# Optimization experiments

Measured on AMD Instinct MI355X. Metric: run time of the kernel, lower is better.

## Reference

```python
import jax, jax.numpy as jnp
import numpy as np

TOP_K = 2

def setup_inputs() -> dict:
    key = jax.random.key(0)
    ks = jax.random.split(key, 7)
    B, L, D, H, E, S = 2, 2048, 1024, 512, 16, 2048
    s = lambda fan_in: (1.0 / np.sqrt(fan_in)).astype(np.float32)
    return {
        "x": jax.random.normal(ks[0], (B, L, D), jnp.float32),
        "gate_w": jax.random.normal(ks[1], (E, D), jnp.float32) * s(D),
        "w1": jax.random.normal(ks[2], (E, H, D), jnp.float32) * s(D),
        "w2": jax.random.normal(ks[3], (E, D, H), jnp.float32) * s(H),
        "sfc1": jax.random.normal(ks[4], (S, D), jnp.float32) * s(D),
        "sfc2": jax.random.normal(ks[5], (S, D), jnp.float32) * s(D),
        "sfc3": jax.random.normal(ks[6], (D, S), jnp.float32) * s(S),
    }

def reference(x, gate_w, w1, w2, sfc1, sfc2, sfc3):
    B, L, D = x.shape
    E = gate_w.shape[0]
    # shared expert: SwiGLU MLP
    shared = jnp.einsum("bls,ds->bld", jax.nn.silu(jnp.einsum("bld,sd->bls", x, sfc1)) * jnp.einsum("bld,sd->bls", x, sfc2), sfc3)
    # router: top-k over gate logits, softmax over selected logits only
    logits = jnp.einsum("bld,ed->ble", x, gate_w)
    top_w, top_idx = jax.lax.top_k(logits, TOP_K)           # [B,L,K]
    top_w = jax.nn.softmax(top_w, axis=-1)
    xf = x.reshape(-1, D)                                    # [T,D]
    T = xf.shape[0]
    idx = top_idx.reshape(T, TOP_K)
    wk = top_w.reshape(T, TOP_K)
    # dense combine weights [T,E]: routing weight where selected, else 0
    dispatch = jnp.zeros((T, E), xf.dtype).at[jnp.arange(T)[:, None], idx].add(wk)
    # all-expert dense compute, combined with dispatch weights (avoids [T,E,D])
    h = jax.nn.silu(jnp.einsum("td,ehd->teh", xf, w1))       # [T,E,H]
    moe = jnp.einsum("teh,te,edh->td", h, dispatch, w2)      # [T,D]
    return moe.reshape(B, L, D) + shared
```

## Files before the change

### kernel.cpp

```cpp
#include <hip/hip_runtime.h>
#include <stdint.h>

#define T_TOK 4096
#define D_DIM 1024
#define H_DIM 512
#define E_NUM 16
#define S_DIM 2048

#define DUAL_BLOCKS 512
#define MOE1_TILES_MAX 80
#define SHOUT_BLOCKS 256

typedef __attribute__((ext_vector_type(8))) __bf16 bf16x8;
typedef __attribute__((ext_vector_type(4))) float f32x4;

__device__ __forceinline__ uint16_t f2bf(float f) {
  uint32_t u = __float_as_uint(f);
  u += 0x7fffu + ((u >> 16) & 1u);
  return (uint16_t)(u >> 16);
}

__device__ __forceinline__ float bf2f(uint16_t u) {
  return __uint_as_float(((uint32_t)u) << 16);
}

__device__ __forceinline__ float silu_f(float v) {
  return v / (1.f + __expf(-v));
}

#define N4_X (T_TOK * D_DIM / 4)
#define N4_S (S_DIM * D_DIM / 4)
#define N4_W (E_NUM * H_DIM * D_DIM / 4)
#define N4_TOT (N4_X + 3 * N4_S + 2 * N4_W)

__global__ __launch_bounds__(256) void k_cast_all(
    const float* __restrict__ x, const float* __restrict__ sfc1,
    const float* __restrict__ sfc2, const float* __restrict__ sfc3,
    const float* __restrict__ w1, const float* __restrict__ w2,
    uint16_t* __restrict__ xb, uint16_t* __restrict__ s1b,
    uint16_t* __restrict__ s2b, uint16_t* __restrict__ s3b,
    uint16_t* __restrict__ w1b, uint16_t* __restrict__ w2b) {
  int i = blockIdx.x * 256 + threadIdx.x;
  if (i >= N4_TOT) return;
  const float* src; uint16_t* dst; int off;
  if (i < N4_X)                    { src = x;    dst = xb;  off = 0; }
  else if (i < N4_X + N4_S)        { src = sfc1; dst = s1b; off = N4_X; }
  else if (i < N4_X + 2 * N4_S)    { src = sfc2; dst = s2b; off = N4_X + N4_S; }
  else if (i < N4_X + 3 * N4_S)    { src = sfc3; dst = s3b; off = N4_X + 2 * N4_S; }
  else if (i < N4_X + 3 * N4_S + N4_W) { src = w1; dst = w1b; off = N4_X + 3 * N4_S; }
  else                             { src = w2;  dst = w2b; off = N4_X + 3 * N4_S + N4_W; }
  int j = i - off;
  float4 v = ((const float4*)src)[j];
  ushort4 o;
  o.x = f2bf(v.x); o.y = f2bf(v.y); o.z = f2bf(v.z); o.w = f2bf(v.w);
  ((ushort4*)dst)[j] = o;
}

__global__ void k_gwT(const float* __restrict__ gw, float4* __restrict__ gwT4) {
  int tid = blockIdx.x * 256 + threadIdx.x;
  if (tid >= E_NUM * (D_DIM / 4)) return;
  int k4 = tid & (D_DIM / 4 - 1);
  int e = tid >> 8;
  float4 v = ((const float4*)(gw + (size_t)e * D_DIM))[k4];
  gwT4[(size_t)k4 * E_NUM + e] = v;
}

__global__ __launch_bounds__(256) void k_router(
    const float* __restrict__ x, const float4* __restrict__ gwT4,
    int* __restrict__ top_idx, float* __restrict__ top_w) {
  const int wid = threadIdx.x >> 6, lane = threadIdx.x & 63;
  const int t = blockIdx.x * 4 + wid;
  const int e = lane & 15, q = lane >> 4;
  const float4* xr4 = (const float4*)(x + (size_t)t * D_DIM) + q * 64;
  const float4* g4 = gwT4 + (size_t)q * 64 * E_NUM + e;
  float acc = 0.f;
#pragma unroll 8
  for (int i = 0; i < 64; i++) {
    float4 xv = xr4[i];
    float4 gv = g4[(size_t)i * E_NUM];
    acc += xv.x * gv.x + xv.y * gv.y + xv.z * gv.z + xv.w * gv.w;
  }
  acc += __shfl_xor(acc, 16, 64);
  acc += __shfl_xor(acc, 32, 64);
  float v1 = acc; int i1 = e;
#pragma unroll
  for (int off = 1; off < 16; off <<= 1) {
    float ov = __shfl_xor(v1, off, 64);
    int oi = __shfl_xor(i1, off, 64);
    if (ov > v1 || (ov == v1 && oi < i1)) { v1 = ov; i1 = oi; }
  }
  float v2 = (e == i1) ? -1e30f : acc; int i2 = e;
#pragma unroll
  for (int off = 1; off < 16; off <<= 1) {
    float ov = __shfl_xor(v2, off, 64);
    int oi = __shfl_xor(i2, off, 64);
    if (ov > v2 || (ov == v2 && oi < i2)) { v2 = ov; i2 = oi; }
  }
  if (lane == 0) {
    float w0 = 1.f / (1.f + __expf(v2 - v1));
    top_idx[t * 2] = i1; top_idx[t * 2 + 1] = i2;
    top_w[t * 2] = w0;  top_w[t * 2 + 1] = 1.f - w0;
  }
}

__global__ __launch_bounds__(256) void k_hist(const int* __restrict__ top_idx,
                                              int* __restrict__ partial) {
  __shared__ int h[E_NUM];
  int tid = threadIdx.x;
  if (tid < E_NUM) h[tid] = 0;
  __syncthreads();
  int id = blockIdx.x * 256 + tid;
  atomicAdd(&h[top_idx[id]], 1);
  __syncthreads();
  if (tid < E_NUM) partial[blockIdx.x * E_NUM + tid] = h[tid];
}

__global__ void k_scan(const int* __restrict__ partial, int* __restrict__ bases,
                       int* __restrict__ offsets, int* __restrict__ tile_e,
                       int* __restrict__ tile_m, int* __restrict__ tile_cnt) {
  __shared__ int tot[E_NUM];
  int e = threadIdx.x;
  if (e < E_NUM) {
    int run = 0;
    for (int b = 0; b < 32; b++) { bases[b * E_NUM + e] = run; run += partial[b * E_NUM + e]; }
    tot[e] = run;
  }
  __syncthreads();
  if (e == 0) {
    int s = 0;
    for (int i = 0; i < E_NUM; i++) { offsets[i] = s; s += tot[i]; }
    offsets[E_NUM] = s;
    int cnt = 0;
    for (int i = 0; i < E_NUM; i++)
      for (int m0 = 0; m0 < tot[i]; m0 += 128) { tile_e[cnt] = i; tile_m[cnt] = m0; cnt++; }
    tile_cnt[0] = cnt;
  }
  __syncthreads();
  if (e < E_NUM) {
    int off = offsets[e];
    for (int b = 0; b < 32; b++) bases[b * E_NUM + e] += off;
  }
}

__global__ __launch_bounds__(256) void k_scatter(
    const int* __restrict__ top_idx, const float* __restrict__ top_w,
    const int* __restrict__ bases, int* __restrict__ slot_token,
    float* __restrict__ slot_w, int* __restrict__ slot_of) {
  __shared__ int cur[E_NUM];
  int tid = threadIdx.x;
  if (tid < E_NUM) cur[tid] = bases[blockIdx.x * E_NUM + tid];
  __syncthreads();
  int id = blockIdx.x * 256 + tid;
  int e = top_idx[id];
  int slot = atomicAdd(&cur[e], 1);
  slot_token[slot] = id >> 1;
  slot_w[slot] = top_w[id];
  slot_of[id] = slot;
}

__global__ __launch_bounds__(256) void k_stage1(
    const uint16_t* __restrict__ xb, const uint16_t* __restrict__ b1,
    const uint16_t* __restrict__ b2, uint16_t* __restrict__ hs,
    const uint16_t* __restrict__ w1b, const int* __restrict__ offsets,
    const int* __restrict__ slot_token, const int* __restrict__ tile_e,
    const int* __restrict__ tile_m, const int* __restrict__ tile_cnt,
    uint16_t* __restrict__ hbuf) {
  __shared__ uint16_t smem[6 * 4096];
  const int bid = blockIdx.x;
  const int tid = threadIdx.x, lane = tid & 63, wid = tid >> 6;
  const int wm = wid >> 1, wn = wid & 1;
  const int r = lane & 15, q = lane >> 4;
  const int row0 = tid >> 2, col8 = (tid & 3) * 8;
  const int st0 = tid * 8, st1 = 2048 + tid * 8;

  if (bid < DUAL_BLOCKS) {
    const int bn0 = (bid & 15) * 128, bm0 = (bid >> 4) * 128;
    uint16_t* sA = smem;
    uint16_t* sB1 = smem + 8192;
    uint16_t* sB2 = smem + 16384;
    f32x4 acc1[4][4], acc2[4][4];
#pragma unroll
    for (int i = 0; i < 4; i++)
#pragma unroll
      for (int j = 0; j < 4; j++) {
        acc1[i][j] = (f32x4){0.f, 0.f, 0.f, 0.f};
        acc2[i][j] = (f32x4){0.f, 0.f, 0.f, 0.f};
      }
    const uint16_t* ga0 = xb + (size_t)(bm0 + row0) * D_DIM + col8;
    const uint16_t* ga1 = ga0 + 64 * D_DIM;
    const uint16_t* gb10 = b1 + (size_t)(bn0 + row0) * D_DIM + col8;
    const uint16_t* gb11 = gb10 + 64 * D_DIM;
    const uint16_t* gb20 = b2 + (size_t)(bn0 + row0) * D_DIM + col8;
    const uint16_t* gb21 = gb20 + 64 * D_DIM;

    uint4 pA0, pA1, pB10, pB11, pB20, pB21;
    pA0 = *(const uint4*)ga0;   pA1 = *(const uint4*)ga1;
    pB10 = *(const uint4*)gb10; pB11 = *(const uint4*)gb11;
    pB20 = *(const uint4*)gb20; pB21 = *(const uint4*)gb21;
    ga0 += 32; ga1 += 32; gb10 += 32; gb11 += 32; gb20 += 32; gb21 += 32;
    *(uint4*)(sA + st0) = pA0;   *(uint4*)(sA + st1) = pA1;
    *(uint4*)(sB1 + st0) = pB10; *(uint4*)(sB1 + st1) = pB11;
    *(uint4*)(sB2 + st0) = pB20; *(uint4*)(sB2 + st1) = pB21;
    __syncthreads();

    int cur = 0;
    for (int kt = 32; kt < D_DIM; kt += 32) {
      pA0 = *(const uint4*)ga0;   pA1 = *(const uint4*)ga1;
      pB10 = *(const uint4*)gb10; pB11 = *(const uint4*)gb11;
      pB20 = *(const uint4*)gb20; pB21 = *(const uint4*)gb21;
      ga0 += 32; ga1 += 32; gb10 += 32; gb11 += 32; gb20 += 32; gb21 += 32;
      {
        const uint16_t* A = sA + cur * 4096;
        const uint16_t* B1 = sB1 + cur * 4096;
        const uint16_t* B2 = sB2 + cur * 4096;
        bf16x8 a[4];
#pragma unroll
        for (int i = 0; i < 4; i++)
          a[i] = *(const bf16x8*)(A + (wm * 64 + i * 16 + r) * 32 + q * 8);
#pragma unroll
        for (int j = 0; j < 4; j++) {
          bf16x8 b = *(const bf16x8*)(B1 + (wn * 64 + j * 16 + r) * 32 + q * 8);
#pragma unroll
          for (int i = 0; i < 4; i++)
            acc1[i][j] = __builtin_amdgcn_mfma_f32_16x16x32_bf16(a[i], b, acc1[i][j], 0, 0, 0);
        }
#pragma unroll
        for (int j = 0; j < 4; j++) {
          bf16x8 b = *(const bf16x8*)(B2 + (wn * 64 + j * 16 + r) * 32 + q * 8);
#pragma unroll
          for (int i = 0; i < 4; i++)
            acc2[i][j] = __builtin_amdgcn_mfma_f32_16x16x32_bf16(a[i], b, acc2[i][j], 0, 0, 0);
        }
      }
      int nxt = cur ^ 1;
      *(uint4*)(sA + nxt * 4096 + st0) = pA0;   *(uint4*)(sA + nxt * 4096 + st1) = pA1;
      *(uint4*)(sB1 + nxt * 4096 + st0) = pB10; *(uint4*)(sB1 + nxt * 4096 + st1) = pB11;
      *(uint4*)(sB2 + nxt * 4096 + st0) = pB20; *(uint4*)(sB2 + nxt * 4096 + st1) = pB21;
      __syncthreads();
      cur = nxt;
    }
    {
      const uint16_t* A = sA + cur * 4096;
      const uint16_t* B1 = sB1 + cur * 4096;
      const uint16_t* B2 = sB2 + cur * 4096;
      bf16x8 a[4];
#pragma unroll
      for (int i = 0; i < 4; i++)
        a[i] = *(const bf16x8*)(A + (wm * 64 + i * 16 + r) * 32 + q * 8);
#pragma unroll
      for (int j = 0; j < 4; j++) {
        bf16x8 b = *(const bf16x8*)(B1 + (wn * 64 + j * 16 + r) * 32 + q * 8);
#pragma unroll
        for (int i = 0; i < 4; i++)
          acc1[i][j] = __builtin_amdgcn_mfma_f32_16x16x32_bf16(a[i], b, acc1[i][j], 0, 0, 0);
      }
#pragma unroll
      for (int j = 0; j < 4; j++) {
        bf16x8 b = *(const bf16x8*)(B2 + (wn * 64 + j * 16 + r) * 32 + q * 8);
#pragma unroll
        for (int i = 0; i < 4; i++)
          acc2[i][j] = __builtin_amdgcn_mfma_f32_16x16x32_bf16(a[i], b, acc2[i][j], 0, 0, 0);
      }
    }
#pragma unroll
    for (int i = 0; i < 4; i++)
#pragma unroll
      for (int j = 0; j < 4; j++)
#pragma unroll
        for (int rr = 0; rr < 4; rr++) {
          int row = bm0 + wm * 64 + i * 16 + q * 4 + rr;
          int col = bn0 + wn * 64 + j * 16 + r;
          hs[(size_t)row * S_DIM + col] = f2bf(silu_f(acc1[i][j][rr]) * acc2[i][j][rr]);
        }
  } else {
    int idx = bid - DUAL_BLOCKS;
    int t = idx >> 2;
    if (t >= tile_cnt[0]) return;
    const int n0 = (idx & 3) * 128;
    const int e = tile_e[t], m0 = tile_m[t];
    const int base = offsets[e];
    const int ne = offsets[e + 1] - base;
    uint16_t* sA = smem;
    uint16_t* sB = smem + 8192;
    f32x4 acc[4][4];
#pragma unroll
    for (int i = 0; i < 4; i++)
#pragma unroll
      for (int j = 0; j < 4; j++) acc[i][j] = (f32x4){0.f, 0.f, 0.f, 0.f};
    const int e0 = min(m0 + row0, ne - 1);
    const int e1 = min(m0 + row0 + 64, ne - 1);
    const uint16_t* ga0 = xb + (size_t)slot_token[base + e0] * D_DIM + col8;
    const uint16_t* ga1 = xb + (size_t)slot_token[base + e1] * D_DIM + col8;
    const uint16_t* wbase = w1b + (size_t)e * H_DIM * D_DIM;
    const uint16_t* gb0 = wbase + (size_t)(n0 + row0) * D_DIM + col8;
    const uint16_t* gb1 = gb0 + 64 * D_DIM;

    uint4 pA0, pA1, pB0, pB1;
    pA0 = *(const uint4*)ga0; pA1 = *(const uint4*)ga1;
    pB0 = *(const uint4*)gb0; pB1 = *(const uint4*)gb1;
    ga0 += 32; ga1 += 32; gb0 += 32; gb1 += 32;
    *(uint4*)(sA + st0) = pA0; *(uint4*)(sA + st1) = pA1;
    *(uint4*)(sB + st0) = pB0; *(uint4*)(sB + st1) = pB1;
    __syncthreads();

    int cur = 0;
    for (int kt = 32; kt < D_DIM; kt += 32) {
      pA0 = *(const uint4*)ga0; pA1 = *(const uint4*)ga1;
      pB0 = *(const uint4*)gb0; pB1 = *(const uint4*)gb1;
      ga0 += 32; ga1 += 32; gb0 += 32; gb1 += 32;
      {
        const uint16_t* A = sA + cur * 4096;
        const uint16_t* B = sB + cur * 4096;
        bf16x8 a[4], bb[4];
#pragma unroll
        for (int i = 0; i < 4; i++)
          a[i] = *(const bf16x8*)(A + (wm * 64 + i * 16 + r) * 32 + q * 8);
#pragma unroll
        for (int j = 0; j < 4; j++)
          bb[j] = *(const bf16x8*)(B + (wn * 64 + j * 16 + r) * 32 + q * 8);
#pragma unroll
        for (int i = 0; i < 4; i++)
#pragma unroll
          for (int j = 0; j < 4; j++)
            acc[i][j] = __builtin_amdgcn_mfma_f32_16x16x32_bf16(a[i], bb[j], acc[i][j], 0, 0, 0);
      }
      int nxt = cur ^ 1;
      *(uint4*)(sA + nxt * 4096 + st0) = pA0; *(uint4*)(sA + nxt * 4096 + st1) = pA1;
      *(uint4*)(sB + nxt * 4096 + st0) = pB0; *(uint4*)(sB + nxt * 4096 + st1) = pB1;
      __syncthreads();
      cur = nxt;
    }
    {
      const uint16_t* A = sA + cur * 4096;
      const uint16_t* B = sB + cur * 4096;
      bf16x8 a[4], bb[4];
#pragma unroll
      for (int i = 0; i < 4; i++)
        a[i] = *(const bf16x8*)(A + (wm * 64 + i * 16 + r) * 32 + q * 8);
#pragma unroll
      for (int j = 0; j < 4; j++)
        bb[j] = *(const bf16x8*)(B + (wn * 64 + j * 16 + r) * 32 + q * 8);
#pragma unroll
      for (int i = 0; i < 4; i++)
#pragma unroll
        for (int j = 0; j < 4; j++)
          acc[i][j] = __builtin_amdgcn_mfma_f32_16x16x32_bf16(a[i], bb[j], acc[i][j], 0, 0, 0);
    }
#pragma unroll
    for (int i = 0; i < 4; i++)
#pragma unroll
      for (int j = 0; j < 4; j++)
#pragma unroll
        for (int rr = 0; rr < 4; rr++) {
          int ent = m0 + wm * 64 + i * 16 + q * 4 + rr;
          if (ent < ne) {
            int col = n0 + wn * 64 + j * 16 + r;
            hbuf[(size_t)(base + ent) * H_DIM + col] = f2bf(silu_f(acc[i][j][rr]));
          }
        }
  }
}

__global__ __launch_bounds__(256) void k_stage2(
    const uint16_t* __restrict__ hsb, const uint16_t* __restrict__ sfc3b,
    float* __restrict__ out, const uint16_t* __restrict__ hbuf,
    const uint16_t* __restrict__ w2b, const int* __restrict__ offsets,
    const float* __restrict__ slot_w, const int* __restrict__ tile_e,
    const int* __restrict__ tile_m, const int* __restrict__ tile_cnt,
    uint16_t* __restrict__ slot_out) {
  __shared__ uint16_t smem[4 * 4096];
  const int bid = blockIdx.x;
  const int tid = threadIdx.x, lane = tid & 63, wid = tid >> 6;
  const int wm = wid >> 1, wn = wid & 1;
  const int r = lane & 15, q = lane >> 4;
  const int row0 = tid >> 2, col8 = (tid & 3) * 8;
  const int st0 = tid * 8, st1 = 2048 + tid * 8;
  uint16_t* sA = smem;
  uint16_t* sB = smem + 8192;

  if (bid < SHOUT_BLOCKS) {
    const int bn0 = (bid & 7) * 128, bm0 = (bid >> 3) * 128;
    f32x4 acc[4][4];
#pragma unroll
    for (int i = 0; i < 4; i++)
#pragma unroll
      for (int j = 0; j < 4; j++) acc[i][j] = (f32x4){0.f, 0.f, 0.f, 0.f};
    const uint16_t* ga0 = hsb + (size_t)(bm0 + row0) * S_DIM + col8;
    const uint16_t* ga1 = ga0 + (size_t)64 * S_DIM;
    const uint16_t* gb0 = sfc3b + (size_t)(bn0 + row0) * S_DIM + col8;
    const uint16_t* gb1 = gb0 + (size_t)64 * S_DIM;

    uint4 pA0, pA1, pB0, pB1;
    pA0 = *(const uint4*)ga0; pA1 = *(const uint4*)ga1;
    pB0 = *(const uint4*)gb0; pB1 = *(const uint4*)gb1;
    ga0 += 32; ga1 += 32; gb0 += 32; gb1 += 32;
    *(uint4*)(sA + st0) = pA0; *(uint4*)(sA + st1) = pA1;
    *(uint4*)(sB + st0) = pB0; *(uint4*)(sB + st1) = pB1;
    __syncthreads();

    int cur = 0;
    for (int kt = 32; kt < S_DIM; kt += 32) {
      pA0 = *(const uint4*)ga0; pA1 = *(const uint4*)ga1;
      pB0 = *(const uint4*)gb0; pB1 = *(const uint4*)gb1;
      ga0 += 32; ga1 += 32; gb0 += 32; gb1 += 32;
      {
        const uint16_t* A = sA + cur * 4096;
        const uint16_t* B = sB + cur * 4096;
        bf16x8 a[4], bb[4];
#pragma unroll
        for (int i = 0; i < 4; i++)
          a[i] = *(const bf16x8*)(A + (wm * 64 + i * 16 + r) * 32 + q * 8);
#pragma unroll
        for (int j = 0; j < 4; j++)
          bb[j] = *(const bf16x8*)(B + (wn * 64 + j * 16 + r) * 32 + q * 8);
#pragma unroll
        for (int i = 0; i < 4; i++)
#pragma unroll
          for (int j = 0; j < 4; j++)
            acc[i][j] = __builtin_amdgcn_mfma_f32_16x16x32_bf16(a[i], bb[j], acc[i][j], 0, 0, 0);
      }
      int nxt = cur ^ 1;
      *(uint4*)(sA + nxt * 4096 + st0) = pA0; *(uint4*)(sA + nxt * 4096 + st1) = pA1;
      *(uint4*)(sB + nxt * 4096 + st0) = pB0; *(uint4*)(sB + nxt * 4096 + st1) = pB1;
      __syncthreads();
      cur = nxt;
    }
    {
      const uint16_t* A = sA + cur * 4096;
      const uint16_t* B = sB + cur * 4096;
      bf16x8 a[4], bb[4];
#pragma unroll
      for (int i = 0; i < 4; i++)
        a[i] = *(const bf16x8*)(A + (wm * 64 + i * 16 + r) * 32 + q * 8);
#pragma unroll
      for (int j = 0; j < 4; j++)
        bb[j] = *(const bf16x8*)(B + (wn * 64 + j * 16 + r) * 32 + q * 8);
#pragma unroll
      for (int i = 0; i < 4; i++)
#pragma unroll
        for (int j = 0; j < 4; j++)
          acc[i][j] = __builtin_amdgcn_mfma_f32_16x16x32_bf16(a[i], bb[j], acc[i][j], 0, 0, 0);
    }
#pragma unroll
    for (int i = 0; i < 4; i++)
#pragma unroll
      for (int j = 0; j < 4; j++)
#pragma unroll
        for (int rr = 0; rr < 4; rr++) {
          int row = bm0 + wm * 64 + i * 16 + q * 4 + rr;
          int col = bn0 + wn * 64 + j * 16 + r;
          out[(size_t)row * D_DIM + col] = acc[i][j][rr];
        }
  } else {
    int idx = bid - SHOUT_BLOCKS;
    int t = idx >> 3;
    if (t >= tile_cnt[0]) return;
    const int n0 = (idx & 7) * 128;
    const int e = tile_e[t], m0 = tile_m[t];
    const int base = offsets[e];
    const int ne = offsets[e + 1] - base;
    f32x4 acc[4][4];
#pragma unroll
    for (int i = 0; i < 4; i++)
#pragma unroll
      for (int j = 0; j < 4; j++) acc[i][j] = (f32x4){0.f, 0.f, 0.f, 0.f};
    const int e0 = min(m0 + row0, ne - 1);
    const int e1 = min(m0 + row0 + 64, ne - 1);
    const uint16_t* ga0 = hbuf + (size_t)(base + e0) * H_DIM + col8;
    const uint16_t* ga1 = hbuf + (size_t)(base + e1) * H_DIM + col8;
    const uint16_t* wbase = w2b + (size_t)e * D_DIM * H_DIM;
    const uint16_t* gb0 = wbase + (size_t)(n0 + row0) * H_DIM + col8;
    const uint16_t* gb1 = gb0 + 64 * H_DIM;

    uint4 pA0, pA1, pB0, pB1;
    pA0 = *(const uint4*)ga0; pA1 = *(const uint4*)ga1;
    pB0 = *(const uint4*)gb0; pB1 = *(const uint4*)gb1;
    ga0 += 32; ga1 += 32; gb0 += 32; gb1 += 32;
    *(uint4*)(sA + st0) = pA0; *(uint4*)(sA + st1) = pA1;
    *(uint4*)(sB + st0) = pB0; *(uint4*)(sB + st1) = pB1;
    __syncthreads();

    int cur = 0;
    for (int kt = 32; kt < H_DIM; kt += 32) {
      pA0 = *(const uint4*)ga0; pA1 = *(const uint4*)ga1;
      pB0 = *(const uint4*)gb0; pB1 = *(const uint4*)gb1;
      ga0 += 32; ga1 += 32; gb0 += 32; gb1 += 32;
      {
        const uint16_t* A = sA + cur * 4096;
        const uint16_t* B = sB + cur * 4096;
        bf16x8 a[4], bb[4];
#pragma unroll
        for (int i = 0; i < 4; i++)
          a[i] = *(const bf16x8*)(A + (wm * 64 + i * 16 + r) * 32 + q * 8);
#pragma unroll
        for (int j = 0; j < 4; j++)
          bb[j] = *(const bf16x8*)(B + (wn * 64 + j * 16 + r) * 32 + q * 8);
#pragma unroll
        for (int i = 0; i < 4; i++)
#pragma unroll
          for (int j = 0; j < 4; j++)
            acc[i][j] = __builtin_amdgcn_mfma_f32_16x16x32_bf16(a[i], bb[j], acc[i][j], 0, 0, 0);
      }
      int nxt = cur ^ 1;
      *(uint4*)(sA + nxt * 4096 + st0) = pA0; *(uint4*)(sA + nxt * 4096 + st1) = pA1;
      *(uint4*)(sB + nxt * 4096 + st0) = pB0; *(uint4*)(sB + nxt * 4096 + st1) = pB1;
      __syncthreads();
      cur = nxt;
    }
    {
      const uint16_t* A = sA + cur * 4096;
      const uint16_t* B = sB + cur * 4096;
      bf16x8 a[4], bb[4];
#pragma unroll
      for (int i = 0; i < 4; i++)
        a[i] = *(const bf16x8*)(A + (wm * 64 + i * 16 + r) * 32 + q * 8);
#pragma unroll
      for (int j = 0; j < 4; j++)
        bb[j] = *(const bf16x8*)(B + (wn * 64 + j * 16 + r) * 32 + q * 8);
#pragma unroll
      for (int i = 0; i < 4; i++)
#pragma unroll
        for (int j = 0; j < 4; j++)
          acc[i][j] = __builtin_amdgcn_mfma_f32_16x16x32_bf16(a[i], bb[j], acc[i][j], 0, 0, 0);
    }
#pragma unroll
    for (int i = 0; i < 4; i++) {
      int ent_base = m0 + wm * 64 + i * 16 + q * 4;
#pragma unroll
      for (int rr = 0; rr < 4; rr++) {
        int ent = ent_base + rr;
        if (ent < ne) {
          float w = slot_w[base + ent];
          uint16_t* orow = slot_out + (size_t)(base + ent) * D_DIM;
#pragma unroll
          for (int j = 0; j < 4; j++) {
            int col = n0 + wn * 64 + j * 16 + r;
            orow[col] = f2bf(w * acc[i][j][rr]);
          }
        }
      }
    }
  }
}

__global__ __launch_bounds__(256) void k_combine(
    const uint16_t* __restrict__ slot_out, const int* __restrict__ slot_of,
    float* __restrict__ out) {
  int t = blockIdx.x;
  int c = threadIdx.x;
  int s0 = slot_of[t * 2], s1 = slot_of[t * 2 + 1];
  ushort4 a = ((const ushort4*)(slot_out + (size_t)s0 * D_DIM))[c];
  ushort4 b = ((const ushort4*)(slot_out + (size_t)s1 * D_DIM))[c];
  float4* po = (float4*)(out + (size_t)t * D_DIM) + c;
  float4 o = *po;
  o.x += bf2f(a.x) + bf2f(b.x);
  o.y += bf2f(a.y) + bf2f(b.y);
  o.z += bf2f(a.z) + bf2f(b.z);
  o.w += bf2f(a.w) + bf2f(b.w);
  *po = o;
}

extern "C" void kernel_launch(void* const* d_in, const int* in_sizes, int n_in,
                              void* d_out, int out_size, void* d_ws, size_t ws_size,
                              hipStream_t stream) {
  const float* x     = (const float*)d_in[0];
  const float* gatew = (const float*)d_in[1];
  const float* w1    = (const float*)d_in[2];
  const float* w2    = (const float*)d_in[3];
  const float* sfc1  = (const float*)d_in[4];
  const float* sfc2  = (const float*)d_in[5];
  const float* sfc3  = (const float*)d_in[6];
  float* out = (float*)d_out;

  uint8_t* ws = (uint8_t*)d_ws;
  size_t off = 0;
  auto alloc = [&](size_t bytes) {
    void* p = ws + off;
    off = (off + bytes + 255) & ~(size_t)255;
    return p;
  };
  uint16_t* xb    = (uint16_t*)alloc((size_t)T_TOK * D_DIM * 2);
  uint16_t* sfc1b = (uint16_t*)alloc((size_t)S_DIM * D_DIM * 2);
  uint16_t* sfc2b = (uint16_t*)alloc((size_t)S_DIM * D_DIM * 2);
  uint16_t* sfc3b = (uint16_t*)alloc((size_t)D_DIM * S_DIM * 2);
  uint16_t* w1b   = (uint16_t*)alloc((size_t)E_NUM * H_DIM * D_DIM * 2);
  uint16_t* w2b   = (uint16_t*)alloc((size_t)E_NUM * D_DIM * H_DIM * 2);
  uint16_t* hsb   = (uint16_t*)alloc((size_t)T_TOK * S_DIM * 2);
  uint16_t* hbuf  = (uint16_t*)alloc((size_t)2 * T_TOK * H_DIM * 2);
  uint16_t* slot_out = (uint16_t*)alloc((size_t)2 * T_TOK * D_DIM * 2);
  float4* gwT4    = (float4*)alloc((size_t)D_DIM / 4 * E_NUM * 16);
  int*   top_idx  = (int*)alloc((size_t)T_TOK * 2 * 4);
  float* top_w    = (float*)alloc((size_t)T_TOK * 2 * 4);
  int*   partial  = (int*)alloc(32 * E_NUM * 4);
  int*   bases    = (int*)alloc(32 * E_NUM * 4);
  int*   offsets  = (int*)alloc((E_NUM + 1) * 4);
  int*   tile_e   = (int*)alloc(MOE1_TILES_MAX * 4);
  int*   tile_m   = (int*)alloc(MOE1_TILES_MAX * 4);
  int*   tile_cnt = (int*)alloc(4);
  int*   slot_token = (int*)alloc((size_t)2 * T_TOK * 4);
  float* slot_w   = (float*)alloc((size_t)2 * T_TOK * 4);
  int*   slot_of  = (int*)alloc((size_t)2 * T_TOK * 4);

  k_cast_all<<<(N4_TOT + 255) / 256, 256, 0, stream>>>(
      x, sfc1, sfc2, sfc3, w1, w2, xb, sfc1b, sfc2b, sfc3b, w1b, w2b);
  k_gwT<<<(E_NUM * D_DIM / 4 + 255) / 256, 256, 0, stream>>>(gatew, gwT4);
  k_router<<<T_TOK / 4, 256, 0, stream>>>(x, gwT4, top_idx, top_w);
  k_hist<<<32, 256, 0, stream>>>(top_idx, partial);
  k_scan<<<1, 64, 0, stream>>>(partial, bases, offsets, tile_e, tile_m, tile_cnt);
  k_scatter<<<32, 256, 0, stream>>>(top_idx, top_w, bases, slot_token, slot_w, slot_of);
  k_stage1<<<DUAL_BLOCKS + MOE1_TILES_MAX * 4, 256, 0, stream>>>(
      xb, sfc1b, sfc2b, hsb, w1b, offsets, slot_token, tile_e, tile_m, tile_cnt, hbuf);
  k_stage2<<<SHOUT_BLOCKS + MOE1_TILES_MAX * 8, 256, 0, stream>>>(
      hsb, sfc3b, out, hbuf, w2b, offsets, slot_w, tile_e, tile_m, tile_cnt, slot_out);
  k_combine<<<T_TOK, 256, 0, stream>>>(slot_out, slot_of, out);
}
```

Before: 311.1 us.

## Switch GEMMs to 32x32x16 MFMA and merge routing prep kernels

All GEMM paths move from 16x16x32 MFMA tiles to 32x32x16 MFMA with f32x16 accumulators. Each warp now loads fewer LDS fragments per MFMA, and the tail iteration is folded into the main loop. The gate-weight transpose is merged into the cast kernel, and hist/scan/scatter are replaced by a single-block sort kernel, which removes several launches. The cost is that the sort now runs serially in one block. Stage2's shared-expert and MoE branches are unified into one loop.

```diff
diff --git a/kernel.cpp b/kernel.cpp
--- a/kernel.cpp
+++ b/kernel.cpp
@@ -12,7 +12,7 @@
 #define SHOUT_BLOCKS 256
 
 typedef __attribute__((ext_vector_type(8))) __bf16 bf16x8;
-typedef __attribute__((ext_vector_type(4))) float f32x4;
+typedef __attribute__((ext_vector_type(16))) float f32x16;
 
 __device__ __forceinline__ uint16_t f2bf(float f) {
   uint32_t u = __float_as_uint(f);
@@ -32,16 +32,27 @@
 #define N4_S (S_DIM * D_DIM / 4)
 #define N4_W (E_NUM * H_DIM * D_DIM / 4)
 #define N4_TOT (N4_X + 3 * N4_S + 2 * N4_W)
+#define N4_GW (E_NUM * D_DIM / 4)
 
 __global__ __launch_bounds__(256) void k_cast_all(
     const float* __restrict__ x, const float* __restrict__ sfc1,
     const float* __restrict__ sfc2, const float* __restrict__ sfc3,
     const float* __restrict__ w1, const float* __restrict__ w2,
+    const float* __restrict__ gw,
     uint16_t* __restrict__ xb, uint16_t* __restrict__ s1b,
     uint16_t* __restrict__ s2b, uint16_t* __restrict__ s3b,
-    uint16_t* __restrict__ w1b, uint16_t* __restrict__ w2b) {
+    uint16_t* __restrict__ w1b, uint16_t* __restrict__ w2b,
+    float4* __restrict__ gwT4) {
   int i = blockIdx.x * 256 + threadIdx.x;
-  if (i >= N4_TOT) return;
+  if (i >= N4_TOT) {
+    int t = i - N4_TOT;
+    if (t < N4_GW) {
+      int k4 = t & (D_DIM / 4 - 1);
+      int e = t >> 8;
+      gwT4[(size_t)k4 * E_NUM + e] = ((const float4*)(gw + (size_t)e * D_DIM))[k4];
+    }
+    return;
+  }
   const float* src; uint16_t* dst; int off;
   if (i < N4_X)                    { src = x;    dst = xb;  off = 0; }
   else if (i < N4_X + N4_S)        { src = sfc1; dst = s1b; off = N4_X; }
@@ -54,15 +65,6 @@
   ushort4 o;
   o.x = f2bf(v.x); o.y = f2bf(v.y); o.z = f2bf(v.z); o.w = f2bf(v.w);
   ((ushort4*)dst)[j] = o;
-}
-
-__global__ void k_gwT(const float* __restrict__ gw, float4* __restrict__ gwT4) {
-  int tid = blockIdx.x * 256 + threadIdx.x;
-  if (tid >= E_NUM * (D_DIM / 4)) return;
-  int k4 = tid & (D_DIM / 4 - 1);
-  int e = tid >> 8;
-  float4 v = ((const float4*)(gw + (size_t)e * D_DIM))[k4];
-  gwT4[(size_t)k4 * E_NUM + e] = v;
 }
 
 __global__ __launch_bounds__(256) void k_router(
@@ -103,60 +105,41 @@
   }
 }
 
-__global__ __launch_bounds__(256) void k_hist(const int* __restrict__ top_idx,
-                                              int* __restrict__ partial) {
+__global__ __launch_bounds__(256) void k_sort(
+    const int* __restrict__ top_idx, const float* __restrict__ top_w,
+    int* __restrict__ offsets, int* __restrict__ tile_e,
+    int* __restrict__ tile_m, int* __restrict__ tile_cnt,
+    int* __restrict__ slot_token, float* __restrict__ slot_w,
+    int* __restrict__ slot_of) {
   __shared__ int h[E_NUM];
+  __shared__ int offs[E_NUM + 1];
   int tid = threadIdx.x;
   if (tid < E_NUM) h[tid] = 0;
   __syncthreads();
-  int id = blockIdx.x * 256 + tid;
-  atomicAdd(&h[top_idx[id]], 1);
+  for (int i = tid; i < 2 * T_TOK; i += 256) atomicAdd(&h[top_idx[i]], 1);
   __syncthreads();
-  if (tid < E_NUM) partial[blockIdx.x * E_NUM + tid] = h[tid];
-}
-
-__global__ void k_scan(const int* __restrict__ partial, int* __restrict__ bases,
-                       int* __restrict__ offsets, int* __restrict__ tile_e,
-                       int* __restrict__ tile_m, int* __restrict__ tile_cnt) {
-  __shared__ int tot[E_NUM];
-  int e = threadIdx.x;
-  if (e < E_NUM) {
-    int run = 0;
-    for (int b = 0; b < 32; b++) { bases[b * E_NUM + e] = run; run += partial[b * E_NUM + e]; }
-    tot[e] = run;
+  if (tid == 0) {
+    int s = 0;
+    for (int e = 0; e < E_NUM; e++) { offs[e] = s; s += h[e]; }
+    offs[E_NUM] = s;
+    int cnt = 0;
+    for (int e = 0; e < E_NUM; e++)
+      for (int m0 = 0; m0 < h[e]; m0 += 128) { tile_e[cnt] = e; tile_m[cnt] = m0; cnt++; }
+    tile_cnt[0] = cnt;
+    for (int e = 0; e <= E_NUM; e++) offsets[e] = offs[e];
   }
   __syncthreads();
-  if (e == 0) {
-    int s = 0;
-    for (int i = 0; i < E_NUM; i++) { offsets[i] = s; s += tot[i]; }
-    offsets[E_NUM] = s;
-    int cnt = 0;
-    for (int i = 0; i < E_NUM; i++)
-      for (int m0 = 0; m0 < tot[i]; m0 += 128) { tile_e[cnt] = i; tile_m[cnt] = m0; cnt++; }
-    tile_cnt[0] = cnt;
-  }
+  if (tid < E_NUM) h[tid] = offs[tid];
   __syncthreads();
-  if (e < E_NUM) {
-    int off = offsets[e];
-    for (int b = 0; b < 32; b++) bases[b * E_NUM + e] += off;
-  }
-}
-
-__global__ __launch_bounds__(256) void k_scatter(
-    const int* __restrict__ top_idx, const float* __restrict__ top_w,
-    const int* __restrict__ bases, int* __restrict__ slot_token,
-    float* __restrict__ slot_w, int* __restrict__ slot_of) {
-  __shared__ int cur[E_NUM];
-  int tid = threadIdx.x;
-  if (tid < E_NUM) cur[tid] = bases[blockIdx.x * E_NUM + tid];
-  __syncthreads();
-  int id = blockIdx.x * 256 + tid;
-  int e = top_idx[id];
-  int slot = atomicAdd(&cur[e], 1);
-  slot_token[slot] = id >> 1;
-  slot_w[slot] = top_w[id];
-  slot_of[id] = slot;
-}
+  for (int i = tid; i < 2 * T_TOK; i += 256) {
+    int e = top_idx[i];
+    int slot = atomicAdd(&h[e], 1);
+    slot_token[slot] = i >> 1;
+    slot_w[slot] = top_w[i];
+    slot_of[i] = slot;
+  }
+}
+
 
 __global__ __launch_bounds__(256) void k_stage1(
     const uint16_t* __restrict__ xb, const uint16_t* __restrict__ b1,
@@ -169,7 +152,7 @@
   const int bid = blockIdx.x;
   const int tid = threadIdx.x, lane = tid & 63, wid = tid >> 6;
   const int wm = wid >> 1, wn = wid & 1;
-  const int r = lane & 15, q = lane >> 4;
+  const int m32 = lane & 31, kh = lane >> 5;
   const int row0 = tid >> 2, col8 = (tid & 3) * 8;
   const int st0 = tid * 8, st1 = 2048 + tid * 8;
 
@@ -178,13 +161,13 @@
     uint16_t* sA = smem;
     uint16_t* sB1 = smem + 8192;
     uint16_t* sB2 = smem + 16384;
-    f32x4 acc1[4][4], acc2[4][4];
-#pragma unroll
-    for (int i = 0; i < 4; i++)
-#pragma unroll
-      for (int j = 0; j < 4; j++) {
-        acc1[i][j] = (f32x4){0.f, 0.f, 0.f, 0.f};
-        acc2[i][j] = (f32x4){0.f, 0.f, 0.f, 0.f};
+    f32x16 acc1[2][2], acc2[2][2];
+#pragma unroll
+    for (int i = 0; i < 2; i++)
+#pragma unroll
+      for (int j = 0; j < 2; j++) {
+        acc1[i][j] = (f32x16)(0.f);
+        acc2[i][j] = (f32x16)(0.f);
       }
     const uint16_t* ga0 = xb + (size_t)(bm0 + row0) * D_DIM + col8;
     const uint16_t* ga1 = ga0 + 64 * D_DIM;
@@ -204,73 +187,56 @@
     __syncthreads();
 
     int cur = 0;
-    for (int kt = 32; kt < D_DIM; kt += 32) {
-      pA0 = *(const uint4*)ga0;   pA1 = *(const uint4*)ga1;
-      pB10 = *(const uint4*)gb10; pB11 = *(const uint4*)gb11;
-      pB20 = *(const uint4*)gb20; pB21 = *(const uint4*)gb21;
-      ga0 += 32; ga1 += 32; gb10 += 32; gb11 += 32; gb20 += 32; gb21 += 32;
+    for (int kt = 32; kt <= D_DIM; kt += 32) {
+      if (kt < D_DIM) {
+        pA0 = *(const uint4*)ga0;   pA1 = *(const uint4*)ga1;
+        pB10 = *(const uint4*)gb10; pB11 = *(const uint4*)gb11;
+        pB20 = *(const uint4*)gb20; pB21 = *(const uint4*)gb21;
+        ga0 += 32; ga1 += 32; gb10 += 32; gb11 += 32; gb20 += 32; gb21 += 32;
+      }
       {
         const uint16_t* A = sA + cur * 4096;
         const uint16_t* B1 = sB1 + cur * 4096;
         const uint16_t* B2 = sB2 + cur * 4096;
-        bf16x8 a[4];
-#pragma unroll
-        for (int i = 0; i < 4; i++)
-          a[i] = *(const bf16x8*)(A + (wm * 64 + i * 16 + r) * 32 + q * 8);
-#pragma unroll
-        for (int j = 0; j < 4; j++) {
-          bf16x8 b = *(const bf16x8*)(B1 + (wn * 64 + j * 16 + r) * 32 + q * 8);
-#pragma unroll
-          for (int i = 0; i < 4; i++)
-            acc1[i][j] = __builtin_amdgcn_mfma_f32_16x16x32_bf16(a[i], b, acc1[i][j], 0, 0, 0);
+#pragma unroll
+        for (int ks = 0; ks < 2; ks++) {
+          const int ko = ks * 16 + kh * 8;
+          bf16x8 a[2], u[2], v[2];
+#pragma unroll
+          for (int i = 0; i < 2; i++)
+            a[i] = *(const bf16x8*)(A + (wm * 64 + i * 32 + m32) * 32 + ko);
+#pragma unroll
+          for (int j = 0; j < 2; j++) {
+            u[j] = *(const bf16x8*)(B1 + (wn * 64 + j * 32 + m32) * 32 + ko);
+            v[j] = *(const bf16x8*)(B2 + (wn * 64 + j * 32 + m32) * 32 + ko);
+          }
+#pragma unroll
+          for (int i = 0; i < 2; i++)
+#pragma unroll
+            for (int j = 0; j < 2; j++) {
+              acc1[i][j] = __builtin_amdgcn_mfma_f32_32x32x16_bf16(a[i], u[j], acc1[i][j], 0, 0, 0);
+              acc2[i][j] = __builtin_amdgcn_mfma_f32_32x32x16_bf16(a[i], v[j], acc2[i][j], 0, 0, 0);
+            }
         }
-#pragma unroll
-        for (int j = 0; j < 4; j++) {
-          bf16x8 b = *(const bf16x8*)(B2 + (wn * 64 + j * 16 + r) * 32 + q * 8);
-#pragma unroll
-          for (int i = 0; i < 4; i++)
-            acc2[i][j] = __builtin_amdgcn_mfma_f32_16x16x32_bf16(a[i], b, acc2[i][j], 0, 0, 0);
-        }
-      }
-      int nxt = cur ^ 1;
-      *(uint4*)(sA + nxt * 4096 + st0) = pA0;   *(uint4*)(sA + nxt * 4096 + st1) = pA1;
-      *(uint4*)(sB1 + nxt * 4096 + st0) = pB10; *(uint4*)(sB1 + nxt * 4096 + st1) = pB11;
-      *(uint4*)(sB2 + nxt * 4096 + st0) = pB20; *(uint4*)(sB2 + nxt * 4096 + st1) = pB21;
-      __syncthreads();
-      cur = nxt;
+      }
+      if (kt < D_DIM) {
+        int nxt = cur ^ 1;
+        *(uint4*)(sA + nxt * 4096 + st0) = pA0;   *(uint4*)(sA + nxt * 4096 + st1) = pA1;
+        *(uint4*)(sB1 + nxt * 4096 + st0) = pB10; *(uint4*)(sB1 + nxt * 4096 + st1) = pB11;
+        *(uint4*)(sB2 + nxt * 4096 + st0) = pB20; *(uint4*)(sB2 + nxt * 4096 + st1) = pB21;
+        __syncthreads();
+        cur = nxt;
+      }
     }
-    {
-      const uint16_t* A = sA + cur * 4096;
-      const uint16_t* B1 = sB1 + cur * 4096;
-      const uint16_t* B2 = sB2 + cur * 4096;
-      bf16x8 a[4];
-#pragma unroll
-      for (int i = 0; i < 4; i++)
-        a[i] = *(const bf16x8*)(A + (wm * 64 + i * 16 + r) * 32 + q * 8);
-#pragma unroll
-      for (int j = 0; j < 4; j++) {
-        bf16x8 b = *(const bf16x8*)(B1 + (wn * 64 + j * 16 + r) * 32 + q * 8);
-#pragma unroll
-        for (int i = 0; i < 4; i++)
-          acc1[i][j] = __builtin_amdgcn_mfma_f32_16x16x32_bf16(a[i], b, acc1[i][j], 0, 0, 0);
-      }
-#pragma unroll
-      for (int j = 0; j < 4; j++) {
-        bf16x8 b = *(const bf16x8*)(B2 + (wn * 64 + j * 16 + r) * 32 + q * 8);
-#pragma unroll
-        for (int i = 0; i < 4; i++)
-          acc2[i][j] = __builtin_amdgcn_mfma_f32_16x16x32_bf16(a[i], b, acc2[i][j], 0, 0, 0);
-      }
-    }
-#pragma unroll
-    for (int i = 0; i < 4; i++)
-#pragma unroll
-      for (int j = 0; j < 4; j++)
-#pragma unroll
-        for (int rr = 0; rr < 4; rr++) {
-          int row = bm0 + wm * 64 + i * 16 + q * 4 + rr;
-          int col = bn0 + wn * 64 + j * 16 + r;
-          hs[(size_t)row * S_DIM + col] = f2bf(silu_f(acc1[i][j][rr]) * acc2[i][j][rr]);
+#pragma unroll
+    for (int i = 0; i < 2; i++)
+#pragma unroll
+      for (int j = 0; j < 2; j++)
+#pragma unroll
+        for (int reg = 0; reg < 16; reg++) {
+          int row = bm0 + wm * 64 + i * 32 + (reg & 3) + 8 * (reg >> 2) + 4 * kh;
+          int col = bn0 + wn * 64 + j * 32 + m32;
+          hs[(size_t)row * S_DIM + col] = f2bf(silu_f(acc1[i][j][reg]) * acc2[i][j][reg]);
         }
   } else {
     int idx = bid - DUAL_BLOCKS;
@@ -282,11 +248,11 @@
     const int ne = offsets[e + 1] - base;
     uint16_t* sA = smem;
     uint16_t* sB = smem + 8192;
-    f32x4 acc[4][4];
-#pragma unroll
-    for (int i = 0; i < 4; i++)
-#pragma unroll
-      for (int j = 0; j < 4; j++) acc[i][j] = (f32x4){0.f, 0.f, 0.f, 0.f};
+    f32x16 acc[2][2];
+#pragma unroll
+    for (int i = 0; i < 2; i++)
+#pragma unroll
+      for (int j = 0; j < 2; j++) acc[i][j] = (f32x16)(0.f);
     const int e0 = min(m0 + row0, ne - 1);
     const int e1 = min(m0 + row0 + 64, ne - 1);
     const uint16_t* ga0 = xb + (size_t)slot_token[base + e0] * D_DIM + col8;
@@ -304,58 +270,50 @@
     __syncthreads();
 
     int cur = 0;
-    for (int kt = 32; kt < D_DIM; kt += 32) {
-      pA0 = *(const uint4*)ga0; pA1 = *(const uint4*)ga1;
-      pB0 = *(const uint4*)gb0; pB1 = *(const uint4*)gb1;
-      ga0 += 32; ga1 += 32; gb0 += 32; gb1 += 32;
+    for (int kt = 32; kt <= D_DIM; kt += 32) {
+      if (kt < D_DIM) {
+        pA0 = *(const uint4*)ga0; pA1 = *(const uint4*)ga1;
+        pB0 = *(const uint4*)gb0; pB1 = *(const uint4*)gb1;
+        ga0 += 32; ga1 += 32; gb0 += 32; gb1 += 32;
+      }
       {
         const uint16_t* A = sA + cur * 4096;
         const uint16_t* B = sB + cur * 4096;
-        bf16x8 a[4], bb[4];
-#pragma unroll
-        for (int i = 0; i < 4; i++)
-          a[i] = *(const bf16x8*)(A + (wm * 64 + i * 16 + r) * 32 + q * 8);
-#pragma unroll
-        for (int j = 0; j < 4; j++)
-          bb[j] = *(const bf16x8*)(B + (wn * 64 + j * 16 + r) * 32 + q * 8);
-#pragma unroll
-        for (int i = 0; i < 4; i++)
-#pragma unroll
-          for (int j = 0; j < 4; j++)
-            acc[i][j] = __builtin_amdgcn_mfma_f32_16x16x32_bf16(a[i], bb[j], acc[i][j], 0, 0, 0);
-      }
-      int nxt = cur ^ 1;
-      *(uint4*)(sA + nxt * 4096 + st0) = pA0; *(uint4*)(sA + nxt * 4096 + st1) = pA1;
-      *(uint4*)(sB + nxt * 4096 + st0) = pB0; *(uint4*)(sB + nxt * 4096 + st1) = pB1;
-      __syncthreads();
-      cur = nxt;
+#pragma unroll
+        for (int ks = 0; ks < 2; ks++) {
+          const int ko = ks * 16 + kh * 8;
+          bf16x8 a[2], bb[2];
+#pragma unroll
+          for (int i = 0; i < 2; i++)
+            a[i] = *(const bf16x8*)(A + (wm * 64 + i * 32 + m32) * 32 + ko);
+#pragma unroll
+          for (int j = 0; j < 2; j++)
+            bb[j] = *(const bf16x8*)(B + (wn * 64 + j * 32 + m32) * 32 + ko);
+#pragma unroll
+          for (int i = 0; i < 2; i++)
+#pragma unroll
+            for (int j = 0; j < 2; j++)
+              acc[i][j] = __builtin_amdgcn_mfma_f32_32x32x16_bf16(a[i], bb[j], acc[i][j], 0, 0, 0);
+        }
+      }
+      if (kt < D_DIM) {
+        int nxt = cur ^ 1;
+        *(uint4*)(sA + nxt * 4096 + st0) = pA0; *(uint4*)(sA + nxt * 4096 + st1) = pA1;
+        *(uint4*)(sB + nxt * 4096 + st0) = pB0; *(uint4*)(sB + nxt * 4096 + st1) = pB1;
+        __syncthreads();
+        cur = nxt;
+      }
     }
-    {
-      const uint16_t* A = sA + cur * 4096;
-      const uint16_t* B = sB + cur * 4096;
-      bf16x8 a[4], bb[4];
-#pragma unroll
-      for (int i = 0; i < 4; i++)
-        a[i] = *(const bf16x8*)(A + (wm * 64 + i * 16 + r) * 32 + q * 8);
-#pragma unroll
-      for (int j = 0; j < 4; j++)
-        bb[j] = *(const bf16x8*)(B + (wn * 64 + j * 16 + r) * 32 + q * 8);
-#pragma unroll
-      for (int i = 0; i < 4; i++)
-#pragma unroll
-        for (int j = 0; j < 4; j++)
-          acc[i][j] = __builtin_amdgcn_mfma_f32_16x16x32_bf16(a[i], bb[j], acc[i][j], 0, 0, 0);
-    }
-#pragma unroll
-    for (int i = 0; i < 4; i++)
-#pragma unroll
-      for (int j = 0; j < 4; j++)
-#pragma unroll
-        for (int rr = 0; rr < 4; rr++) {
-          int ent = m0 + wm * 64 + i * 16 + q * 4 + rr;
+#pragma unroll
+    for (int i = 0; i < 2; i++)
+#pragma unroll
+      for (int j = 0; j < 2; j++)
+#pragma unroll
+        for (int reg = 0; reg < 16; reg++) {
+          int ent = m0 + wm * 64 + i * 32 + (reg & 3) + 8 * (reg >> 2) + 4 * kh;
           if (ent < ne) {
-            int col = n0 + wn * 64 + j * 16 + r;
-            hbuf[(size_t)(base + ent) * H_DIM + col] = f2bf(silu_f(acc[i][j][rr]));
+            int col = n0 + wn * 64 + j * 32 + m32;
+            hbuf[(size_t)(base + ent) * H_DIM + col] = f2bf(silu_f(acc[i][j][reg]));
           }
         }
   }
@@ -372,174 +330,118 @@
   const int bid = blockIdx.x;
   const int tid = threadIdx.x, lane = tid & 63, wid = tid >> 6;
   const int wm = wid >> 1, wn = wid & 1;
-  const int r = lane & 15, q = lane >> 4;
+  const int m32 = lane & 31, kh = lane >> 5;
   const int row0 = tid >> 2, col8 = (tid & 3) * 8;
   const int st0 = tid * 8, st1 = 2048 + tid * 8;
   uint16_t* sA = smem;
   uint16_t* sB = smem + 8192;
 
-  if (bid < SHOUT_BLOCKS) {
-    const int bn0 = (bid & 7) * 128, bm0 = (bid >> 3) * 128;
-    f32x4 acc[4][4];
-#pragma unroll
-    for (int i = 0; i < 4; i++)
-#pragma unroll
-      for (int j = 0; j < 4; j++) acc[i][j] = (f32x4){0.f, 0.f, 0.f, 0.f};
-    const uint16_t* ga0 = hsb + (size_t)(bm0 + row0) * S_DIM + col8;
-    const uint16_t* ga1 = ga0 + (size_t)64 * S_DIM;
-    const uint16_t* gb0 = sfc3b + (size_t)(bn0 + row0) * S_DIM + col8;
-    const uint16_t* gb1 = gb0 + (size_t)64 * S_DIM;
-
-    uint4 pA0, pA1, pB0, pB1;
-    pA0 = *(const uint4*)ga0; pA1 = *(const uint4*)ga1;
-    pB0 = *(const uint4*)gb0; pB1 = *(const uint4*)gb1;
-    ga0 += 32; ga1 += 32; gb0 += 32; gb1 += 32;
-    *(uint4*)(sA + st0) = pA0; *(uint4*)(sA + st1) = pA1;
-    *(uint4*)(sB + st0) = pB0; *(uint4*)(sB + st1) = pB1;
-    __syncthreads();
-
-    int cur = 0;
-    for (int kt = 32; kt < S_DIM; kt += 32) {
+  f32x16 acc[2][2];
+#pragma unroll
+  for (int i = 0; i < 2; i++)
+#pragma unroll
+    for (int j = 0; j < 2; j++) acc[i][j] = (f32x16)(0.f);
+
+  const uint16_t *ga0, *ga1, *gb0, *gb1;
+  int kiters;
+  int bm0 = 0, bn0 = 0, base = 0, ne = 0, m0 = 0, n0 = 0;
+  bool is_shout = (bid < SHOUT_BLOCKS);
+  if (is_shout) {
+    bn0 = (bid & 7) * 128; bm0 = (bid >> 3) * 128;
+    ga0 = hsb + (size_t)(bm0 + row0) * S_DIM + col8;
+    ga1 = ga0 + (size_t)64 * S_DIM;
+    gb0 = sfc3b + (size_t)(bn0 + row0) * S_DIM + col8;
+    gb1 = gb0 + (size_t)64 * S_DIM;
+    kiters = S_DIM / 32;
+  } else {
+    int idx = bid - SHOUT_BLOCKS;
+    int t = idx >> 3;
+    if (t >= tile_cnt[0]) return;
+    n0 = (idx & 7) * 128;
+    int e = tile_e[t]; m0 = tile_m[t];
+    base = offsets[e];
+    ne = offsets[e + 1] - base;
+    const int e0 = min(m0 + row0, ne - 1);
+    const int e1 = min(m0 + row0 + 64, ne - 1);
+    ga0 = hbuf + (size_t)(base + e0) * H_DIM + col8;
+    ga1 = hbuf + (size_t)(base + e1) * H_DIM + col8;
+    const uint16_t* wbase = w2b + (size_t)e * D_DIM * H_DIM;
+    gb0 = wbase + (size_t)(n0 + row0) * H_DIM + col8;
+    gb1 = gb0 + 64 * H_DIM;
+    kiters = H_DIM / 32;
+  }
+
+  uint4 pA0, pA1, pB0, pB1;
+  pA0 = *(const uint4*)ga0; pA1 = *(const uint4*)ga1;
+  pB0 = *(const uint4*)gb0; pB1 = *(const uint4*)gb1;
+  ga0 += 32; ga1 += 32; gb0 += 32; gb1 += 32;
+  *(uint4*)(sA + st0) = pA0; *(uint4*)(sA + st1) = pA1;
+  *(uint4*)(sB + st0) = pB0; *(uint4*)(sB + st1) = pB1;
+  __syncthreads();
+
+  int cur = 0;
+  for (int kt = 1; kt <= kiters; kt++) {
+    if (kt < kiters) {
       pA0 = *(const uint4*)ga0; pA1 = *(const uint4*)ga1;
       pB0 = *(const uint4*)gb0; pB1 = *(const uint4*)gb1;
       ga0 += 32; ga1 += 32; gb0 += 32; gb1 += 32;
-      {
-        const uint16_t* A = sA + cur * 4096;
-        const uint16_t* B = sB + cur * 4096;
-        bf16x8 a[4], bb[4];
-#pragma unroll
-        for (int i = 0; i < 4; i++)
-          a[i] = *(const bf16x8*)(A + (wm * 64 + i * 16 + r) * 32 + q * 8);
-#pragma unroll
-        for (int j = 0; j < 4; j++)
-          bb[j] = *(const bf16x8*)(B + (wn * 64 + j * 16 + r) * 32 + q * 8);
-#pragma unroll
-        for (int i = 0; i < 4; i++)
-#pragma unroll
-          for (int j = 0; j < 4; j++)
-            acc[i][j] = __builtin_amdgcn_mfma_f32_16x16x32_bf16(a[i], bb[j], acc[i][j], 0, 0, 0);
-      }
+    }
+    {
+      const uint16_t* A = sA + cur * 4096;
+      const uint16_t* B = sB + cur * 4096;
+#pragma unroll
+      for (int ks = 0; ks < 2; ks++) {
+        const int ko = ks * 16 + kh * 8;
+        bf16x8 a[2], bb[2];
+#pragma unroll
+        for (int i = 0; i < 2; i++)
+          a[i] = *(const bf16x8*)(A + (wm * 64 + i * 32 + m32) * 32 + ko);
+#pragma unroll
+        for (int j = 0; j < 2; j++)
+          bb[j] = *(const bf16x8*)(B + (wn * 64 + j * 32 + m32) * 32 + ko);
+#pragma unroll
+        for (int i = 0; i < 2; i++)
+#pragma unroll
+          for (int j = 0; j < 2; j++)
+            acc[i][j] = __builtin_amdgcn_mfma_f32_32x32x16_bf16(a[i], bb[j], acc[i][j], 0, 0, 0);
+      }
+    }
+    if (kt < kiters) {
       int nxt = cur ^ 1;
       *(uint4*)(sA + nxt * 4096 + st0) = pA0; *(uint4*)(sA + nxt * 4096 + st1) = pA1;
       *(uint4*)(sB + nxt * 4096 + st0) = pB0; *(uint4*)(sB + nxt * 4096 + st1) = pB1;
       __syncthreads();
       cur = nxt;
     }
-    {
-      const uint16_t* A = sA + cur * 4096;
-      const uint16_t* B = sB + cur * 4096;
-      bf16x8 a[4], bb[4];
-#pragma unroll
-      for (int i = 0; i < 4; i++)
-        a[i] = *(const bf16x8*)(A + (wm * 64 + i * 16 + r) * 32 + q * 8);
-#pragma unroll
-      for (int j = 0; j < 4; j++)
-        bb[j] = *(const bf16x8*)(B + (wn * 64 + j * 16 + r) * 32 + q * 8);
-#pragma unroll
-      for (int i = 0; i < 4; i++)
-#pragma unroll
-        for (int j = 0; j < 4; j++)
-          acc[i][j] = __builtin_amdgcn_mfma_f32_16x16x32_bf16(a[i], bb[j], acc[i][j], 0, 0, 0);
-    }
-#pragma unroll
-    for (int i = 0; i < 4; i++)
-#pragma unroll
-      for (int j = 0; j < 4; j++)
-#pragma unroll
-        for (int rr = 0; rr < 4; rr++) {
-          int row = bm0 + wm * 64 + i * 16 + q * 4 + rr;
-          int col = bn0 + wn * 64 + j * 16 + r;
-          out[(size_t)row * D_DIM + col] = acc[i][j][rr];
+  }
+
+  if (is_shout) {
+#pragma unroll
+    for (int i = 0; i < 2; i++)
+#pragma unroll
+      for (int j = 0; j < 2; j++)
+#pragma unroll
+        for (int reg = 0; reg < 16; reg++) {
+          int row = bm0 + wm * 64 + i * 32 + (reg & 3) + 8 * (reg >> 2) + 4 * kh;
+          int col = bn0 + wn * 64 + j * 32 + m32;
+          out[(size_t)row * D_DIM + col] = acc[i][j][reg];
         }
   } else {
-    int idx = bid - SHOUT_BLOCKS;
-    int t = idx >> 3;
-    if (t >= tile_cnt[0]) return;
-    const int n0 = (idx & 7) * 128;
-    const int e = tile_e[t], m0 = tile_m[t];
-    const int base = offsets[e];
-    const int ne = offsets[e + 1] - base;
-    f32x4 acc[4][4];
-#pragma unroll
-    for (int i = 0; i < 4; i++)
-#pragma unroll
-      for (int j = 0; j < 4; j++) acc[i][j] = (f32x4){0.f, 0.f, 0.f, 0.f};
-    const int e0 = min(m0 + row0, ne - 1);
-    const int e1 = min(m0 + row0 + 64, ne - 1);
-    const uint16_t* ga0 = hbuf + (size_t)(base + e0) * H_DIM + col8;
-    const uint16_t* ga1 = hbuf + (size_t)(base + e1) * H_DIM + col8;
-    const uint16_t* wbase = w2b + (size_t)e * D_DIM * H_DIM;
-    const uint16_t* gb0 = wbase + (size_t)(n0 + row0) * H_DIM + col8;
-    const uint16_t* gb1 = gb0 + 64 * H_DIM;
-
-    uint4 pA0, pA1, pB0, pB1;
-    pA0 = *(const uint4*)ga0; pA1 = *(const uint4*)ga1;
-    pB0 = *(const uint4*)gb0; pB1 = *(const uint4*)gb1;
-    ga0 += 32; ga1 += 32; gb0 += 32; gb1 += 32;
-    *(uint4*)(sA + st0) = pA0; *(uint4*)(sA + st1) = pA1;
-    *(uint4*)(sB + st0) = pB0; *(uint4*)(sB + st1) = pB1;
-    __syncthreads();
-
-    int cur = 0;
-    for (int kt = 32; kt < H_DIM; kt += 32) {
-      pA0 = *(const uint4*)ga0; pA1 = *(const uint4*)ga1;
-      pB0 = *(const uint4*)gb0; pB1 = *(const uint4*)gb1;
-      ga0 += 32; ga1 += 32; gb0 += 32; gb1 += 32;
-      {
-        const uint16_t* A = sA + cur * 4096;
-        const uint16_t* B = sB + cur * 4096;
-        bf16x8 a[4], bb[4];
-#pragma unroll
-        for (int i = 0; i < 4; i++)
-          a[i] = *(const bf16x8*)(A + (wm * 64 + i * 16 + r) * 32 + q * 8);
-#pragma unroll
-        for (int j = 0; j < 4; j++)
-          bb[j] = *(const bf16x8*)(B + (wn * 64 + j * 16 + r) * 32 + q * 8);
-#pragma unroll
-        for (int i = 0; i < 4; i++)
-#pragma unroll
-          for (int j = 0; j < 4; j++)
-            acc[i][j] = __builtin_amdgcn_mfma_f32_16x16x32_bf16(a[i], bb[j], acc[i][j], 0, 0, 0);
-      }
-      int nxt = cur ^ 1;
-      *(uint4*)(sA + nxt * 4096 + st0) = pA0; *(uint4*)(sA + nxt * 4096 + st1) = pA1;
-      *(uint4*)(sB + nxt * 4096 + st0) = pB0; *(uint4*)(sB + nxt * 4096 + st1) = pB1;
-      __syncthreads();
-      cur = nxt;
-    }
-    {
-      const uint16_t* A = sA + cur * 4096;
-      const uint16_t* B = sB + cur * 4096;
-      bf16x8 a[4], bb[4];
-#pragma unroll
-      for (int i = 0; i < 4; i++)
-        a[i] = *(const bf16x8*)(A + (wm * 64 + i * 16 + r) * 32 + q * 8);
-#pragma unroll
-      for (int j = 0; j < 4; j++)
-        bb[j] = *(const bf16x8*)(B + (wn * 64 + j * 16 + r) * 32 + q * 8);
-#pragma unroll
-      for (int i = 0; i < 4; i++)
-#pragma unroll
-        for (int j = 0; j < 4; j++)
-          acc[i][j] = __builtin_amdgcn_mfma_f32_16x16x32_bf16(a[i], bb[j], acc[i][j], 0, 0, 0);
-    }
-#pragma unroll
-    for (int i = 0; i < 4; i++) {
-      int ent_base = m0 + wm * 64 + i * 16 + q * 4;
-#pragma unroll
-      for (int rr = 0; rr < 4; rr++) {
-        int ent = ent_base + rr;
+#pragma unroll
+    for (int i = 0; i < 2; i++)
+#pragma unroll
+      for (int reg = 0; reg < 16; reg++) {
+        int ent = m0 + wm * 64 + i * 32 + (reg & 3) + 8 * (reg >> 2) + 4 * kh;
         if (ent < ne) {
           float w = slot_w[base + ent];
           uint16_t* orow = slot_out + (size_t)(base + ent) * D_DIM;
 #pragma unroll
-          for (int j = 0; j < 4; j++) {
-            int col = n0 + wn * 64 + j * 16 + r;
-            orow[col] = f2bf(w * acc[i][j][rr]);
+          for (int j = 0; j < 2; j++) {
+            int col = n0 + wn * 64 + j * 32 + m32;
+            orow[col] = f2bf(w * acc[i][j][reg]);
           }
         }
       }
-    }
   }
 }
 
@@ -591,8 +493,6 @@
   float4* gwT4    = (float4*)alloc((size_t)D_DIM / 4 * E_NUM * 16);
   int*   top_idx  = (int*)alloc((size_t)T_TOK * 2 * 4);
   float* top_w    = (float*)alloc((size_t)T_TOK * 2 * 4);
-  int*   partial  = (int*)alloc(32 * E_NUM * 4);
-  int*   bases    = (int*)alloc(32 * E_NUM * 4);
   int*   offsets  = (int*)alloc((E_NUM + 1) * 4);
   int*   tile_e   = (int*)alloc(MOE1_TILES_MAX * 4);
   int*   tile_m   = (int*)alloc(MOE1_TILES_MAX * 4);
@@ -601,13 +501,12 @@
   float* slot_w   = (float*)alloc((size_t)2 * T_TOK * 4);
   int*   slot_of  = (int*)alloc((size_t)2 * T_TOK * 4);
 
-  k_cast_all<<<(N4_TOT + 255) / 256, 256, 0, stream>>>(
-      x, sfc1, sfc2, sfc3, w1, w2, xb, sfc1b, sfc2b, sfc3b, w1b, w2b);
-  k_gwT<<<(E_NUM * D_DIM / 4 + 255) / 256, 256, 0, stream>>>(gatew, gwT4);
+  k_cast_all<<<(N4_TOT + N4_GW + 255) / 256, 256, 0, stream>>>(
+      x, sfc1, sfc2, sfc3, w1, w2, gatew,
+      xb, sfc1b, sfc2b, sfc3b, w1b, w2b, gwT4);
   k_router<<<T_TOK / 4, 256, 0, stream>>>(x, gwT4, top_idx, top_w);
-  k_hist<<<32, 256, 0, stream>>>(top_idx, partial);
-  k_scan<<<1, 64, 0, stream>>>(partial, bases, offsets, tile_e, tile_m, tile_cnt);
-  k_scatter<<<32, 256, 0, stream>>>(top_idx, top_w, bases, slot_token, slot_w, slot_of);
+  k_sort<<<1, 256, 0, stream>>>(top_idx, top_w, offsets, tile_e, tile_m,
+                                tile_cnt, slot_token, slot_w, slot_of);
   k_stage1<<<DUAL_BLOCKS + MOE1_TILES_MAX * 4, 256, 0, stream>>>(
       xb, sfc1b, sfc2b, hsb, w1b, offsets, slot_token, tile_e, tile_m, tile_cnt, hbuf);
   k_stage2<<<SHOUT_BLOCKS + MOE1_TILES_MAX * 8, 256, 0, stream>>>(
```

Result: slower. 354.8 us (+14.1%).
